# Optimization experiments

Hardware: AMD Instinct MI355X
Metric: run time of the kernel (lower is better)

Reference implementation:

```python
import jax, jax.numpy as jnp
import numpy as np

EMBED = 3072
HEADS = 24
HEAD_DIM = EMBED // HEADS
FFN = 4 * EMBED
SEGS = (1024, 2048, 4096)
DILS = (1, 2, 4)
SEQ = 8192
BATCH = 1


def setup_inputs() -> dict:
    key = jax.random.key(0)
    ks = jax.random.split(key, 8)
    E, F = EMBED, FFN
    s = lambda k, shape, sc: (jax.random.normal(k, shape, jnp.float32) * sc)
    return {
        "x": s(ks[0], (BATCH, SEQ, E), 1.0),
        "expert_embed": s(ks[1], (1, 1, E), 0.02),
        "w_qkv": s(ks[2], (3 * E, E), E ** -0.5),
        "b_qkv": jnp.zeros((3 * E,), jnp.float32),
        "w_out": s(ks[3], (E, E), E ** -0.5),
        "b_out": jnp.zeros((E,), jnp.float32),
        "ln1_g": jnp.ones((E,), jnp.float32),
        "ln1_b": jnp.zeros((E,), jnp.float32),
        "w1": s(ks[4], (F, E), E ** -0.5),
        "b1": jnp.zeros((F,), jnp.float32),
        "w2": s(ks[5], (E, F), F ** -0.5),
        "b2": jnp.zeros((E,), jnp.float32),
        "ln2_g": jnp.ones((E,), jnp.float32),
        "ln2_b": jnp.zeros((E,), jnp.float32),
    }


def _layernorm(x, g, b):
    m = jnp.mean(x, axis=-1, keepdims=True)
    v = jnp.mean(jnp.square(x - m), axis=-1, keepdims=True)
    return (x - m) * jax.lax.rsqrt(v + 1e-5) * g + b


def _dilated_attn(q, k, v):
    # q,k,v: [b, n, h, d]; heads are partitioned across dilation groups
    b, n, h, d = q.shape
    G = len(SEGS)
    hg = h // G
    scale = 1.0 / np.sqrt(d)
    outs = []
    for i, (g, r) in enumerate(zip(SEGS, DILS)):
        off = i % r
        hs = slice(i * hg, (i + 1) * hg)

        def sel(t):
            # [b, n, h, d] -> [b, n//g, g//r, hg, d] (dilated segment view)
            return t.reshape(b, n // g, g, h, d)[:, :, off::r, hs, :]

        qi, ki, vi = sel(q), sel(k), sel(v)
        att = jnp.einsum("bsqhd,bskhd->bshqk", qi, ki) * scale
        att = jax.nn.softmax(att, axis=-1)
        oi = jnp.einsum("bshqk,bskhd->bsqhd", att, vi)
        # scatter dilated positions back; unselected positions stay zero
        buf = jnp.zeros((b, n // g, g, hg, d), q.dtype).at[:, :, off::r].set(oi)
        outs.append(buf.reshape(b, n, hg, d))
    return jnp.concatenate(outs, axis=2)  # head groups are contiguous slices


def reference(x, expert_embed, w_qkv, b_qkv, w_out, b_out,
              ln1_g, ln1_b, w1, b1, w2, b2, ln2_g, ln2_b):
    b, n, E = x.shape
    x = x + expert_embed
    qkv = x @ w_qkv.T + b_qkv
    q, k, v = [t.reshape(b, n, HEADS, HEAD_DIM) for t in jnp.split(qkv, 3, axis=-1)]
    a = _dilated_attn(q, k, v).reshape(b, n, E) @ w_out.T + b_out
    x = _layernorm(x + a, ln1_g, ln1_b)
    f = jax.nn.gelu(x @ w1.T + b1, approximate=False) @ w2.T + b2
    return _layernorm(x + f, ln2_g, ln2_b)
```

## Files before the change

### kernel.cpp

```cpp
#include <hip/hip_runtime.h>

typedef unsigned short u16;
typedef __bf16 bf16x8 __attribute__((ext_vector_type(8)));
typedef float f32x4 __attribute__((ext_vector_type(4)));
typedef u16 u16x4 __attribute__((ext_vector_type(4)));
typedef u16 u16x8 __attribute__((ext_vector_type(8)));

__device__ __forceinline__ u16 f2bf(float f) {
  union { float f; unsigned u; } v; v.f = f;
  return (u16)((v.u + 0x7fffu + ((v.u >> 16) & 1u)) >> 16);
}
__device__ __forceinline__ float b2f(u16 h) {
  union { unsigned u; float f; } v; v.u = ((unsigned)h) << 16; return v.f;
}

__device__ __forceinline__ void gld16(const void* g, void* l) {
  __builtin_amdgcn_global_load_lds(
      (const __attribute__((address_space(1))) unsigned int*)g,
      (__attribute__((address_space(3))) unsigned int*)l, 16, 0, 0);
}

#define BAR() asm volatile("s_barrier" ::: "memory")
#define VMC4() asm volatile("s_waitcnt vmcnt(4)" ::: "memory")
#define VMC3() asm volatile("s_waitcnt vmcnt(3)" ::: "memory")
#define VMC0() asm volatile("s_waitcnt vmcnt(0)" ::: "memory")

__global__ __launch_bounds__(256) void prep_kernel(const float* __restrict__ x,
                                                   const float* __restrict__ ee,
                                                   u16* __restrict__ xb) {
  size_t i = ((size_t)blockIdx.x * 256 + threadIdx.x) * 4;
  int col = (int)(i % 3072);
  f32x4 v = *(const f32x4*)&x[i];
  f32x4 e = *(const f32x4*)&ee[col];
  v += e;
  u16x4 b = { f2bf(v[0]), f2bf(v[1]), f2bf(v[2]), f2bf(v[3]) };
  *(u16x4*)&xb[i] = b;
}

__global__ __launch_bounds__(256) void cvt_kernel(const float* __restrict__ in,
                                                  u16* __restrict__ out, size_t n) {
  size_t i = ((size_t)blockIdx.x * 256 + threadIdx.x) * 4;
  if (i >= n) return;
  f32x4 v = *(const f32x4*)&in[i];
  u16x4 b = { f2bf(v[0]), f2bf(v[1]), f2bf(v[2]), f2bf(v[3]) };
  *(u16x4*)&out[i] = b;
}

__global__ __launch_bounds__(256) void cvt_strided_kernel(const float* __restrict__ in,
                                                          u16* __restrict__ out, int k0) {
  size_t i = ((size_t)blockIdx.x * 256 + threadIdx.x) * 4;
  int n = (int)(i / 6144), k = (int)(i % 6144);
  f32x4 v = *(const f32x4*)&in[(size_t)n * 12288 + k0 + k];
  u16x4 b = { f2bf(v[0]), f2bf(v[1]), f2bf(v[2]), f2bf(v[3]) };
  *(u16x4*)&out[i] = b;
}

template<int EPI>
__global__ __launch_bounds__(512, 2) void gemm8_kernel(const u16* __restrict__ A,
                                                       const u16* __restrict__ B,
                                                       const float* __restrict__ bias,
                                                       void* __restrict__ C0,
                                                       void* __restrict__ C1,
                                                       int N, int K) {
  __shared__ __align__(16) u16 lds[65536];
  const int tid = threadIdx.x;
  const int lane = tid & 63;
  const int w = tid >> 6;
  const int lr = lane & 15, lc8 = (lane >> 4) * 8;
  const int wm128 = (w >> 2) * 128, wn64 = (w & 3) * 64;
  const int rsw = (lr & 7) << 3;

  const int ntile = N >> 8;
  int bid = blockIdx.x;
  int wg = (bid & 7) * (gridDim.x >> 3) + (bid >> 3);
  const int bm = wg / ntile, bn = wg % ntile;
  const size_t m0 = (size_t)bm << 8, n0 = (size_t)bn << 8;

  const int jsw = (tid & 7) ^ ((tid >> 3) & 7);
  const u16* gA = A + (m0 + (tid >> 3)) * (size_t)K + jsw * 8;
  const u16* gB = B + (n0 + ((tid >> 8) << 6) + ((tid >> 3) & 31)) * (size_t)K + jsw * 8;
  u16* lA = &lds[tid * 8];
  u16* lB = &lds[16384 + (((tid >> 8) << 12) | (((tid >> 3) & 31) << 6) | ((tid & 7) << 3))];

  f32x4 acc[8][4] = {};
  bf16x8 af[2][4], bfr[2][2];

  auto stageA = [&](int buf, int mh, int kk) {
    const int ro = mh * 64;
    gld16(gA + (size_t)ro * K + kk, lA + buf * 32768 + ro * 64);
    gld16(gA + (size_t)(ro + 128) * K + kk, lA + buf * 32768 + (ro + 128) * 64);
  };
  auto stageB = [&](int buf, int nh, int kk) {
    const int ro = nh * 32;
    gld16(gB + (size_t)ro * K + kk, lB + buf * 32768 + ro * 64);
    gld16(gB + (size_t)(ro + 128) * K + kk, lB + buf * 32768 + (ro + 128) * 64);
  };
  auto LA = [&](int buf, int mh) {
#pragma unroll
    for (int ks = 0; ks < 2; ++ks)
#pragma unroll
      for (int f = 0; f < 4; ++f) {
        int r = wm128 + mh * 64 + f * 16 + lr;
        af[ks][f] = *(const bf16x8*)&lds[buf * 32768 + r * 64 + ((ks * 32 + lc8) ^ rsw)];
      }
  };
  auto LB = [&](int buf, int nh) {
#pragma unroll
    for (int ks = 0; ks < 2; ++ks)
#pragma unroll
      for (int f = 0; f < 2; ++f) {
        int r = wn64 + nh * 32 + f * 16 + lr;
        bfr[ks][f] = *(const bf16x8*)&lds[buf * 32768 + 16384 + r * 64 + ((ks * 32 + lc8) ^ rsw)];
      }
  };
  auto MMA = [&](int mh, int nh) {
    __builtin_amdgcn_s_setprio(1);
#pragma unroll
    for (int ks = 0; ks < 2; ++ks)
#pragma unroll
      for (int f = 0; f < 4; ++f)
#pragma unroll
        for (int f2 = 0; f2 < 2; ++f2)
          acc[mh * 4 + f][nh * 2 + f2] = __builtin_amdgcn_mfma_f32_16x16x32_bf16(
              af[ks][f], bfr[ks][f2], acc[mh * 4 + f][nh * 2 + f2], 0, 0, 0);
    __builtin_amdgcn_s_setprio(0);
  };

  stageA(0, 0, 0); stageB(0, 1, 0); stageA(0, 1, 0); stageB(0, 0, 0);
  stageA(1, 0, 64); stageB(1, 1, 64);
  VMC4();
  BAR();

  const int NIT = K >> 7;
  for (int it = 0; it < NIT; ++it) {
    const int kk = it << 7;
    const bool pred = (it + 1 < NIT);
    LA(0, 0); LB(0, 0);
    stageA(1, 1, kk + 64);
    BAR(); MMA(0, 0); BAR();
    LB(0, 1);
    stageB(1, 0, kk + 64);
    BAR(); MMA(0, 1); BAR();
    LA(0, 1);
    if (pred) stageA(0, 0, kk + 128);
    BAR(); MMA(1, 1); BAR();
    LB(0, 0);
    if (pred) stageB(0, 1, kk + 128);
    BAR(); MMA(1, 0);
    if (pred) { VMC4(); } else { VMC0(); }
    BAR();
    LA(1, 0); LB(1, 0);
    if (pred) stageA(0, 1, kk + 128);
    BAR(); MMA(0, 0); BAR();
    LB(1, 1);
    if (pred) stageB(0, 0, kk + 128);
    BAR(); MMA(0, 1); BAR();
    LA(1, 1);
    if (pred) stageA(1, 0, kk + 192);
    BAR(); MMA(1, 1); BAR();
    LB(1, 0);
    if (pred) stageB(1, 1, kk + 192);
    BAR(); MMA(1, 0);
    if (pred) { VMC4(); }
    BAR();
  }

#pragma unroll
  for (int ni = 0; ni < 4; ++ni) {
    const int colL = wn64 + ni * 16 + lr;
    const size_t col = n0 + colL;
    const float bv = bias[col];
    const int ci = colL >> 3;
#pragma unroll
    for (int mi = 0; mi < 8; ++mi) {
#pragma unroll
      for (int rg = 0; rg < 4; ++rg) {
        const int rowL = wm128 + mi * 16 + (lc8 >> 1) + rg;
        float v = acc[mi][ni][rg] + bv;
        if constexpr (EPI == 2)
          v = 0.5f * v * (1.0f + erff(v * 0.7071067811865476f));
        const int fz = (rowL >> 2) & 7;
        lds[rowL * 256 + (((ci ^ fz) << 3) | (colL & 7))] = f2bf(v);
      }
    }
  }
  __syncthreads();
  const int row = tid >> 1, half = tid & 1;
  const int fro = (row >> 2) & 7;
  u16* dst;
  size_t cb;
  int ldc;
  if constexpr (EPI == 7) {
    const int sec = (n0 >= 3072);
    dst = sec ? (u16*)C1 : (u16*)C0;
    cb = n0 - (sec ? 3072 : 0);
    ldc = 3072;
  } else {
    dst = (u16*)C0; cb = n0; ldc = N;
  }
  u16* gout = dst + (m0 + row) * (size_t)ldc + cb + half * 128;
#pragma unroll
  for (int i = 0; i < 16; ++i) {
    const int ci = half * 16 + i;
    *(uint4*)&gout[i * 8] = *(const uint4*)&lds[row * 256 + ((ci ^ fro) << 3)];
  }
}

template<int EPI>
__global__ __launch_bounds__(512, 2) void gemm8n_kernel(const u16* __restrict__ A,
                                                        const u16* __restrict__ B,
                                                        const float* __restrict__ bias,
                                                        const float* __restrict__ residf,
                                                        const u16* __restrict__ residb,
                                                        const float* __restrict__ ee,
                                                        void* __restrict__ C0,
                                                        int N, int K) {
  __shared__ __align__(16) u16 lds[49152];
  const int tid = threadIdx.x;
  const int lane = tid & 63;
  const int w = tid >> 6;
  const int lr = lane & 15, lc8 = (lane >> 4) * 8;
  const int wm128 = (w >> 2) * 128;
  const int wn16 = (w & 3) * 16;
  const int rsw = (lr & 7) << 3;

  const int ntile = N >> 7;
  int bid = blockIdx.x;
  int wg = (bid & 7) * (gridDim.x >> 3) + (bid >> 3);
  const int bm = wg / ntile, bn = wg % ntile;
  const size_t m0 = (size_t)bm << 8, n0 = (size_t)bn << 7;

  const int jsw = (tid & 7) ^ ((tid >> 3) & 7);
  const u16* gA = A + (m0 + (tid >> 3)) * (size_t)K + jsw * 8;
  const u16* gB = B + (n0 + (tid >> 3)) * (size_t)K + jsw * 8;
  u16* lA = &lds[tid * 8];
  u16* lB = &lds[16384 + tid * 8];

  f32x4 acc[8][2] = {};
  bf16x8 af[2][4], bfr[2];

  auto stageA = [&](int buf, int mh, int kk) {
    const int ro = mh * 64;
    gld16(gA + (size_t)ro * K + kk, lA + buf * 24576 + ro * 64);
    gld16(gA + (size_t)(ro + 128) * K + kk, lA + buf * 24576 + (ro + 128) * 64);
  };
  auto stageB = [&](int buf, int nh, int kk) {
    gld16(gB + (size_t)(nh * 64) * K + kk, lB + buf * 24576 + nh * 4096);
  };
  auto LA = [&](int buf, int mh) {
#pragma unroll
    for (int ks = 0; ks < 2; ++ks)
#pragma unroll
      for (int f = 0; f < 4; ++f) {
        int r = wm128 + mh * 64 + f * 16 + lr;
        af[ks][f] = *(const bf16x8*)&lds[buf * 24576 + r * 64 + ((ks * 32 + lc8) ^ rsw)];
      }
  };
  auto LB = [&](int buf, int nh) {
#pragma unroll
    for (int ks = 0; ks < 2; ++ks) {
      int r = nh * 64 + wn16 + lr;
      bfr[ks] = *(const bf16x8*)&lds[buf * 24576 + 16384 + r * 64 + ((ks * 32 + lc8) ^ rsw)];
    }
  };
  auto MMA = [&](int mh, int nh) {
    __builtin_amdgcn_s_setprio(1);
#pragma unroll
    for (int ks = 0; ks < 2; ++ks)
#pragma unroll
      for (int f = 0; f < 4; ++f)
        acc[mh * 4 + f][nh] = __builtin_amdgcn_mfma_f32_16x16x32_bf16(
            af[ks][f], bfr[ks], acc[mh * 4 + f][nh], 0, 0, 0);
    __builtin_amdgcn_s_setprio(0);
  };

  stageA(0, 0, 0); stageB(0, 1, 0); stageA(0, 1, 0); stageB(0, 0, 0);
  stageA(1, 0, 64); stageB(1, 1, 64);
  VMC3();
  BAR();

  const int NIT = K >> 7;
  for (int it = 0; it < NIT; ++it) {
    const int kk = it << 7;
    const bool pred = (it + 1 < NIT);
    LA(0, 0); LB(0, 0);
    stageA(1, 1, kk + 64);
    BAR(); MMA(0, 0); BAR();
    LB(0, 1);
    stageB(1, 0, kk + 64);
    BAR(); MMA(0, 1); BAR();
    LA(0, 1);
    if (pred) stageA(0, 0, kk + 128);
    BAR(); MMA(1, 1); BAR();
    LB(0, 0);
    if (pred) stageB(0, 1, kk + 128);
    BAR(); MMA(1, 0);
    if (pred) { VMC3(); } else { VMC0(); }
    BAR();
    LA(1, 0); LB(1, 0);
    if (pred) stageA(0, 1, kk + 128);
    BAR(); MMA(0, 0); BAR();
    LB(1, 1);
    if (pred) stageB(0, 0, kk + 128);
    BAR(); MMA(0, 1); BAR();
    LA(1, 1);
    if (pred) stageA(1, 0, kk + 192);
    BAR(); MMA(1, 1); BAR();
    LB(1, 0);
    if (pred) stageB(1, 1, kk + 192);
    BAR(); MMA(1, 0);
    if (pred) { VMC3(); }
    BAR();
  }

#pragma unroll
  for (int nh = 0; nh < 2; ++nh) {
    const int colL = nh * 64 + wn16 + lr;
    const size_t col = n0 + colL;
    float bv = 0.f;
    if constexpr (EPI != 9) bv = bias[col];
    const int ci = colL >> 3;
#pragma unroll
    for (int mi = 0; mi < 8; ++mi) {
#pragma unroll
      for (int rg = 0; rg < 4; ++rg) {
        const int rowL = wm128 + mi * 16 + (lc8 >> 1) + rg;
        const size_t idx = (m0 + rowL) * (size_t)N + col;
        float v = acc[mi][nh][rg] + bv;
        if constexpr (EPI == 3) v += residf[idx] + ee[col];
        if constexpr (EPI == 8) v += b2f(residb[idx]);
        if constexpr (EPI == 9) v += b2f(((const u16*)C0)[idx]);
        const int fz = (rowL >> 2) & 7;
        lds[rowL * 128 + (((ci ^ fz) << 3) | (colL & 7))] = f2bf(v);
      }
    }
  }
  __syncthreads();
  const int row = tid >> 1, half = tid & 1;
  const int fro = (row >> 2) & 7;
  u16* gout = (u16*)C0 + (m0 + row) * (size_t)N + n0 + half * 64;
#pragma unroll
  for (int i = 0; i < 8; ++i) {
    const int ci = half * 8 + i;
    *(uint4*)&gout[i * 8] = *(const uint4*)&lds[row * 128 + ((ci ^ fro) << 3)];
  }
}

__device__ __forceinline__ void decode_blk(int bid, int& grp, int& g, int& r, int& off,
                                           int& q16, int& hl, int& s) {
  if (bid < 1024)      { grp = 0; g = 1024; r = 1; off = 0; }
  else if (bid < 1536) { grp = 1; g = 2048; r = 2; off = 1; bid -= 1024; }
  else                 { grp = 2; g = 4096; r = 4; off = 2; bid -= 1536; }
  q16 = bid & 15; hl = (bid >> 4) & 7; s = bid >> 7;
}

__global__ __launch_bounds__(256) void vtrans_kernel(const u16* __restrict__ Vb,
                                                     u16* __restrict__ vtd) {
  int grp, g, r, off, jb, hl, s;
  decode_blk(blockIdx.x, grp, g, r, off, jb, hl, s);
  const int h = grp * 8 + hl;
  const size_t vbase = (size_t)((grp == 0) ? 0u : (grp == 1) ? 8388608u : 12582912u)
                       + (size_t)(s * 8 + hl) * 131072;
  __shared__ u16 t[64 * 128];
  const int tid = threadIdx.x;
#pragma unroll
  for (int i = 0; i < 4; ++i) {
    int c = tid + i * 256;
    int jj = c >> 4, c16 = c & 15;
    size_t pos = (size_t)s * g + off + (size_t)(jb * 64 + jj) * r;
    uint4 d = *(const uint4*)&Vb[pos * 3072 + h * 128 + c16 * 8];
    *(uint4*)((char*)t + jj * 256 + ((c16 * 16) ^ ((jj >> 3) << 4))) = d;
  }
  __syncthreads();
#pragma unroll
  for (int i = 0; i < 4; ++i) {
    int c = tid + i * 256;
    int dd = c >> 3, jc = c & 7;
    u16x8 vals;
#pragma unroll
    for (int q = 0; q < 8; ++q) {
      int row = jc * 8 + q;
      vals[q] = *(const u16*)((const char*)t + row * 256 + ((dd * 2) ^ (jc << 4)));
    }
    *(u16x8*)&vtd[vbase + (size_t)dd * 1024 + jb * 64 + jc * 8] = vals;
  }
}

__global__ __launch_bounds__(256) void attn_kernel(const u16* __restrict__ Qb,
                                                   const u16* __restrict__ Kb,
                                                   const u16* __restrict__ vtd,
                                                   u16* __restrict__ abuf) {
  int grp, g, r, off, qt, hl, s;
  decode_blk(blockIdx.x, grp, g, r, off, qt, hl, s);
  const int h = grp * 8 + hl;
  const size_t vbase = (size_t)((grp == 0) ? 0u : (grp == 1) ? 8388608u : 12582912u)
                       + (size_t)(s * 8 + hl) * 131072;
  const size_t segoff = (size_t)s * g + off;

  const int tid = threadIdx.x;
  const int lane = tid & 63, w = tid >> 6;
  const int lr = lane & 15, lc = lane >> 4;

  __shared__ u16 Kl[64 * 128];
  __shared__ u16 Vl[128 * 64];
  __shared__ u16 Pl[4][1024];

  const size_t qpos = segoff + (size_t)(qt * 64 + w * 16 + lr) * r;
  const u16* qrow = &Qb[qpos * 3072 + h * 128];
  bf16x8 qf[4];
#pragma unroll
  for (int kc = 0; kc < 4; ++kc) qf[kc] = *(const bf16x8*)&qrow[kc * 32 + lc * 8];

  float m_run[4], l_run[4];
  f32x4 ao[8] = {};
#pragma unroll
  for (int i = 0; i < 4; ++i) { m_run[i] = -1e30f; l_run[i] = 0.f; }

  const float scale = 0.08838834764831845f;

  for (int kt = 0; kt < 16; ++kt) {
    __syncthreads();
#pragma unroll
    for (int i = 0; i < 4; ++i) {
      int c = tid + i * 256;
      int jj = c >> 4, c16 = c & 15;
      size_t kpos = segoff + (size_t)(kt * 64 + jj) * r;
      uint4 kd = *(const uint4*)&Kb[kpos * 3072 + h * 128 + c16 * 8];
      *(uint4*)((char*)Kl + jj * 256 + ((c16 * 16) ^ ((jj & 7) << 4))) = kd;
      int dd = c >> 3, jc = c & 7;
      uint4 vd = *(const uint4*)&vtd[vbase + (size_t)dd * 1024 + kt * 64 + jc * 8];
      *(uint4*)((char*)Vl + dd * 128 + ((jc * 16) ^ ((dd & 7) << 4))) = vd;
    }
    __syncthreads();

    f32x4 sc4[4] = {};
#pragma unroll
    for (int kb = 0; kb < 4; ++kb) {
      const int key = kb * 16 + lr;
      const int swz = (key & 7) << 4;
#pragma unroll
      for (int kc = 0; kc < 4; ++kc) {
        bf16x8 kf = *(const bf16x8*)((const char*)Kl + key * 256 + ((kc * 64 + lc * 16) ^ swz));
        sc4[kb] = __builtin_amdgcn_mfma_f32_16x16x32_bf16(qf[kc], kf, sc4[kb], 0, 0, 0);
      }
    }

    float pv[4][4];
#pragma unroll
    for (int rg = 0; rg < 4; ++rg) {
      float t = fmaxf(fmaxf(sc4[0][rg], sc4[1][rg]), fmaxf(sc4[2][rg], sc4[3][rg]));
#pragma unroll
      for (int sh = 1; sh < 16; sh <<= 1) t = fmaxf(t, __shfl_xor(t, sh, 64));
      t *= scale;
      const float mn = fmaxf(m_run[rg], t);
      const float corr = __expf(m_run[rg] - mn);
      m_run[rg] = mn;
      float sum = 0.f;
#pragma unroll
      for (int kb = 0; kb < 4; ++kb) {
        float p = __expf(sc4[kb][rg] * scale - mn);
        pv[kb][rg] = p; sum += p;
      }
#pragma unroll
      for (int sh = 1; sh < 16; sh <<= 1) sum += __shfl_xor(sum, sh, 64);
      l_run[rg] = l_run[rg] * corr + sum;
#pragma unroll
      for (int nb = 0; nb < 8; ++nb) ao[nb][rg] *= corr;
    }

#pragma unroll
    for (int rg = 0; rg < 4; ++rg) {
      const int q = lc * 4 + rg;
      const int swq = (q & 7) << 4;
#pragma unroll
      for (int kb = 0; kb < 4; ++kb) {
        const int key = kb * 16 + lr;
        *(u16*)((char*)&Pl[w][0] + q * 128 + ((key * 2) ^ swq)) = f2bf(pv[kb][rg]);
      }
    }
    __syncthreads();

#pragma unroll
    for (int kc2 = 0; kc2 < 2; ++kc2) {
      bf16x8 pf = *(const bf16x8*)((const char*)&Pl[w][0] + lr * 128 + ((kc2 * 64 + lc * 16) ^ ((lr & 7) << 4)));
#pragma unroll
      for (int nb = 0; nb < 8; ++nb) {
        const int dd = nb * 16 + lr;
        bf16x8 vf = *(const bf16x8*)((const char*)Vl + dd * 128 + ((kc2 * 64 + lc * 16) ^ ((dd & 7) << 4)));
        ao[nb] = __builtin_amdgcn_mfma_f32_16x16x32_bf16(pf, vf, ao[nb], 0, 0, 0);
      }
    }
  }

#pragma unroll
  for (int rg = 0; rg < 4; ++rg) {
    const float inv = 1.f / l_run[rg];
    const size_t opos = segoff + (size_t)(qt * 64 + w * 16 + lc * 4 + rg) * r;
    u16* orow = &abuf[opos * 3072 + h * 128];
#pragma unroll
    for (int nb = 0; nb < 8; ++nb) orow[nb * 16 + lr] = f2bf(ao[nb][rg] * inv);
  }
}

template<int IN_BF, int OUT_BF>
__global__ __launch_bounds__(256) void ln_kernel(const void* __restrict__ yv,
                                                 const float* __restrict__ gm,
                                                 const float* __restrict__ bt,
                                                 void* __restrict__ outv) {
  const size_t row = blockIdx.x;
  const int tid = threadIdx.x;
  float v[12];
  float s = 0.f, ss = 0.f;
#pragma unroll
  for (int i = 0; i < 3; ++i) {
    if constexpr (IN_BF) {
      u16x4 raw = *(const u16x4*)((const u16*)yv + row * 3072 + tid * 4 + i * 1024);
#pragma unroll
      for (int j = 0; j < 4; ++j) { float f = b2f(raw[j]); v[i * 4 + j] = f; s += f; ss += f * f; }
    } else {
      f32x4 raw = *(const f32x4*)((const float*)yv + row * 3072 + tid * 4 + i * 1024);
#pragma unroll
      for (int j = 0; j < 4; ++j) { float f = raw[j]; v[i * 4 + j] = f; s += f; ss += f * f; }
    }
  }
#pragma unroll
  for (int sh = 1; sh < 64; sh <<= 1) { s += __shfl_xor(s, sh, 64); ss += __shfl_xor(ss, sh, 64); }
  __shared__ float red[8];
  if ((tid & 63) == 0) { red[tid >> 6] = s; red[4 + (tid >> 6)] = ss; }
  __syncthreads();
  s = red[0] + red[1] + red[2] + red[3];
  ss = red[4] + red[5] + red[6] + red[7];
  const float mean = s * (1.f / 3072.f);
  const float var = ss * (1.f / 3072.f) - mean * mean;
  const float rs = rsqrtf(var + 1e-5f);
#pragma unroll
  for (int i = 0; i < 3; ++i) {
    int c = tid * 4 + i * 1024;
    f32x4 g4 = *(const f32x4*)&gm[c];
    f32x4 b4 = *(const f32x4*)&bt[c];
    if constexpr (OUT_BF) {
      u16x4 ob;
#pragma unroll
      for (int j = 0; j < 4; ++j) ob[j] = f2bf((v[i * 4 + j] - mean) * rs * g4[j] + b4[j]);
      *(u16x4*)((u16*)outv + row * 3072 + c) = ob;
    } else {
      f32x4 o;
#pragma unroll
      for (int j = 0; j < 4; ++j) o[j] = (v[i * 4 + j] - mean) * rs * g4[j] + b4[j];
      *(f32x4*)((float*)outv + row * 3072 + c) = o;
    }
  }
}

extern "C" void kernel_launch(void* const* d_in, const int* in_sizes, int n_in,
                              void* d_out, int out_size, void* d_ws, size_t ws_size,
                              hipStream_t stream) {
  (void)in_sizes; (void)n_in; (void)out_size;
  const float* x    = (const float*)d_in[0];
  const float* ee   = (const float*)d_in[1];
  const float* wqkv = (const float*)d_in[2];
  const float* bqkv = (const float*)d_in[3];
  const float* wout = (const float*)d_in[4];
  const float* bout = (const float*)d_in[5];
  const float* ln1g = (const float*)d_in[6];
  const float* ln1b = (const float*)d_in[7];
  const float* w1   = (const float*)d_in[8];
  const float* b1   = (const float*)d_in[9];
  const float* w2   = (const float*)d_in[10];
  const float* b2   = (const float*)d_in[11];
  const float* ln2g = (const float*)d_in[12];
  const float* ln2b = (const float*)d_in[13];
  float* out = (float*)d_out;

  static const size_t OFF_B1  = 50331648;
  static const size_t OFF_B2  = 100663296;
  static const size_t WS_NEED = 150994944;
  if (ws_size < WS_NEED) return;

  char* ws = (char*)d_ws;
  u16*   xb    = (u16*)(ws);
  u16*   vtd   = (u16*)(ws);
  u16*   wbo   = (u16*)(ws);
  u16*   x1b   = (u16*)(ws);
  u16*   Qb    = (u16*)(ws + OFF_B1);
  u16*   y1b   = (u16*)(ws + OFF_B1);
  u16*   y2b   = (u16*)(ws + OFF_B1);
  u16*   wslot = (u16*)(ws + OFF_B2);
  u16*   abuf  = (u16*)(ws + OFF_B2);
  u16*   Kb    = (u16*)d_out;
  u16*   Vb    = (u16*)((char*)d_out + 50331648);
  u16*   hcd   = (u16*)d_out;

  prep_kernel<<<24576, 256, 0, stream>>>(x, ee, xb);

  cvt_kernel<<<18432, 256, 0, stream>>>(wqkv, wslot, 18874368);
  gemm8_kernel<7><<<768, 512, 0, stream>>>(xb, wslot, bqkv, Qb, Kb, 6144, 3072);
  cvt_kernel<<<9216, 256, 0, stream>>>(wqkv + 18874368, wslot, 9437184);
  gemm8n_kernel<0><<<768, 512, 0, stream>>>(xb, wslot, bqkv + 6144, nullptr, nullptr, nullptr,
                                            Vb, 3072, 3072);

  vtrans_kernel<<<1792, 256, 0, stream>>>(Vb, vtd);
  hipMemsetAsync(abuf, 0, 50331648, stream);
  attn_kernel<<<1792, 256, 0, stream>>>(Qb, Kb, vtd, abuf);

  cvt_kernel<<<9216, 256, 0, stream>>>(wout, wbo, 9437184);
  gemm8n_kernel<3><<<768, 512, 0, stream>>>(abuf, wbo, bout, x, nullptr, ee,
                                            y1b, 3072, 3072);
  ln_kernel<1, 1><<<8192, 256, 0, stream>>>(y1b, ln1g, ln1b, x1b);

  for (int c = 0; c < 2; ++c) {
    cvt_kernel<<<18432, 256, 0, stream>>>(w1 + (size_t)c * 18874368, wslot, 18874368);
    gemm8_kernel<2><<<768, 512, 0, stream>>>(x1b, wslot, b1 + c * 6144, hcd, nullptr, 6144, 3072);
    cvt_strided_kernel<<<18432, 256, 0, stream>>>(w2, wslot, c * 6144);
    if (c == 0)
      gemm8n_kernel<8><<<768, 512, 0, stream>>>(hcd, wslot, b2, nullptr, x1b, nullptr,
                                                y2b, 3072, 6144);
    else
      gemm8n_kernel<9><<<768, 512, 0, stream>>>(hcd, wslot, b2, nullptr, nullptr, nullptr,
                                                y2b, 3072, 6144);
  }

  ln_kernel<1, 0><<<8192, 256, 0, stream>>>(y2b, ln2g, ln2b, out);
}
```

Before: 2.332 ms.

## Triple-buffer the N=3072 GEMM with 64x64 warp tiles and deepen prefetch

The 256x128 GEMM used for the V, out-projection and FFN-down GEMMs is replaced with a three-stage LDS ring buffer over 64-wide K slices. It also moves from 8 warps of 128x16 tiles to 4x2 warps of 64x64 tiles, which raises per-warp fragment reuse. The wider 8-wave GEMM reorders its async staging so one more stage is in flight, waiting at vmcnt(6) instead of vmcnt(4). The aim is to hide global-load latency and cut LDS fragment reloads. The larger LDS allocation (144 KB) likely stops two blocks from fitting per CU, reducing occupancy.

```diff
diff --git a/kernel.cpp b/kernel.cpp
--- a/kernel.cpp
+++ b/kernel.cpp
@@ -21,8 +21,7 @@
 }
 
 #define BAR() asm volatile("s_barrier" ::: "memory")
-#define VMC4() asm volatile("s_waitcnt vmcnt(4)" ::: "memory")
-#define VMC3() asm volatile("s_waitcnt vmcnt(3)" ::: "memory")
+#define VMC6() asm volatile("s_waitcnt vmcnt(6)" ::: "memory")
 #define VMC0() asm volatile("s_waitcnt vmcnt(0)" ::: "memory")
 
 __global__ __launch_bounds__(256) void prep_kernel(const float* __restrict__ x,
@@ -127,8 +126,8 @@
   };
 
   stageA(0, 0, 0); stageB(0, 1, 0); stageA(0, 1, 0); stageB(0, 0, 0);
-  stageA(1, 0, 64); stageB(1, 1, 64);
-  VMC4();
+  stageA(1, 0, 64); stageB(1, 1, 64); stageA(1, 1, 64);
+  VMC6();
   BAR();
 
   const int NIT = K >> 7;
@@ -136,32 +135,32 @@
     const int kk = it << 7;
     const bool pred = (it + 1 < NIT);
     LA(0, 0); LB(0, 0);
-    stageA(1, 1, kk + 64);
+    stageB(1, 0, kk + 64);
     BAR(); MMA(0, 0); BAR();
     LB(0, 1);
-    stageB(1, 0, kk + 64);
+    if (pred) stageA(0, 0, kk + 128);
     BAR(); MMA(0, 1); BAR();
     LA(0, 1);
-    if (pred) stageA(0, 0, kk + 128);
+    if (pred) stageB(0, 1, kk + 128);
     BAR(); MMA(1, 1); BAR();
     LB(0, 0);
-    if (pred) stageB(0, 1, kk + 128);
+    if (pred) stageA(0, 1, kk + 128);
     BAR(); MMA(1, 0);
-    if (pred) { VMC4(); } else { VMC0(); }
+    if (pred) { VMC6(); } else { VMC0(); }
     BAR();
     LA(1, 0); LB(1, 0);
-    if (pred) stageA(0, 1, kk + 128);
+    if (pred) stageB(0, 0, kk + 128);
     BAR(); MMA(0, 0); BAR();
     LB(1, 1);
-    if (pred) stageB(0, 0, kk + 128);
+    if (pred) stageA(1, 0, kk + 192);
     BAR(); MMA(0, 1); BAR();
     LA(1, 1);
-    if (pred) stageA(1, 0, kk + 192);
+    if (pred) stageB(1, 1, kk + 192);
     BAR(); MMA(1, 1); BAR();
     LB(1, 0);
-    if (pred) stageB(1, 1, kk + 192);
+    if (pred) stageA(1, 1, kk + 192);
     BAR(); MMA(1, 0);
-    if (pred) { VMC4(); }
+    if (pred) { VMC6(); }
     BAR();
   }
 
@@ -207,7 +206,7 @@
 }
 
 template<int EPI>
-__global__ __launch_bounds__(512, 2) void gemm8n_kernel(const u16* __restrict__ A,
+__global__ __launch_bounds__(512, 2) void gemm4p_kernel(const u16* __restrict__ A,
                                                         const u16* __restrict__ B,
                                                         const float* __restrict__ bias,
                                                         const float* __restrict__ residf,
@@ -215,13 +214,13 @@
                                                         const float* __restrict__ ee,
                                                         void* __restrict__ C0,
                                                         int N, int K) {
-  __shared__ __align__(16) u16 lds[49152];
+  __shared__ __align__(16) u16 lds[73728];
   const int tid = threadIdx.x;
   const int lane = tid & 63;
   const int w = tid >> 6;
   const int lr = lane & 15, lc8 = (lane >> 4) * 8;
-  const int wm128 = (w >> 2) * 128;
-  const int wn16 = (w & 3) * 16;
+  const int wm64 = (w >> 1) * 64;
+  const int wn64 = (w & 1) * 64;
   const int rsw = (lr & 7) << 3;
 
   const int ntile = N >> 7;
@@ -236,97 +235,89 @@
   u16* lA = &lds[tid * 8];
   u16* lB = &lds[16384 + tid * 8];
 
-  f32x4 acc[8][2] = {};
-  bf16x8 af[2][4], bfr[2];
-
-  auto stageA = [&](int buf, int mh, int kk) {
-    const int ro = mh * 64;
-    gld16(gA + (size_t)ro * K + kk, lA + buf * 24576 + ro * 64);
-    gld16(gA + (size_t)(ro + 128) * K + kk, lA + buf * 24576 + (ro + 128) * 64);
-  };
-  auto stageB = [&](int buf, int nh, int kk) {
-    gld16(gB + (size_t)(nh * 64) * K + kk, lB + buf * 24576 + nh * 4096);
-  };
-  auto LA = [&](int buf, int mh) {
+  f32x4 acc[4][4] = {};
+  bf16x8 af[2][4], bfr[2][2];
+
+  const int NT = K >> 6;
+
+  auto stageA2 = [&](int buf, int kk) {
+    gld16(gA + kk, lA + buf * 24576);
+    gld16(gA + (size_t)128 * K + kk, lA + buf * 24576 + 128 * 64);
+    gld16(gA + (size_t)64 * K + kk, lA + buf * 24576 + 64 * 64);
+    gld16(gA + (size_t)192 * K + kk, lA + buf * 24576 + 192 * 64);
+  };
+  auto stageB1 = [&](int buf, int kk) {
+    gld16(gB + kk, lB + buf * 24576);
+    gld16(gB + (size_t)64 * K + kk, lB + buf * 24576 + 64 * 64);
+  };
+  auto LA = [&](int buf) {
 #pragma unroll
     for (int ks = 0; ks < 2; ++ks)
 #pragma unroll
       for (int f = 0; f < 4; ++f) {
-        int r = wm128 + mh * 64 + f * 16 + lr;
+        int r = wm64 + f * 16 + lr;
         af[ks][f] = *(const bf16x8*)&lds[buf * 24576 + r * 64 + ((ks * 32 + lc8) ^ rsw)];
       }
   };
-  auto LB = [&](int buf, int nh) {
-#pragma unroll
-    for (int ks = 0; ks < 2; ++ks) {
-      int r = nh * 64 + wn16 + lr;
-      bfr[ks] = *(const bf16x8*)&lds[buf * 24576 + 16384 + r * 64 + ((ks * 32 + lc8) ^ rsw)];
-    }
-  };
-  auto MMA = [&](int mh, int nh) {
+  auto LB = [&](int buf, int ch) {
+#pragma unroll
+    for (int ks = 0; ks < 2; ++ks)
+#pragma unroll
+      for (int f2 = 0; f2 < 2; ++f2) {
+        int r = wn64 + ch * 32 + f2 * 16 + lr;
+        bfr[ks][f2] = *(const bf16x8*)&lds[buf * 24576 + 16384 + r * 64 + ((ks * 32 + lc8) ^ rsw)];
+      }
+  };
+  auto MMA = [&](int ch) {
     __builtin_amdgcn_s_setprio(1);
 #pragma unroll
     for (int ks = 0; ks < 2; ++ks)
 #pragma unroll
       for (int f = 0; f < 4; ++f)
-        acc[mh * 4 + f][nh] = __builtin_amdgcn_mfma_f32_16x16x32_bf16(
-            af[ks][f], bfr[ks], acc[mh * 4 + f][nh], 0, 0, 0);
+#pragma unroll
+        for (int f2 = 0; f2 < 2; ++f2)
+          acc[f][ch * 2 + f2] = __builtin_amdgcn_mfma_f32_16x16x32_bf16(
+              af[ks][f], bfr[ks][f2], acc[f][ch * 2 + f2], 0, 0, 0);
     __builtin_amdgcn_s_setprio(0);
   };
-
-  stageA(0, 0, 0); stageB(0, 1, 0); stageA(0, 1, 0); stageB(0, 0, 0);
-  stageA(1, 0, 64); stageB(1, 1, 64);
-  VMC3();
+  auto TILE = [&](int bc, int bs, int tt) {
+    const int kk2 = (tt + 2) << 6;
+    const bool p = (tt + 2) < NT;
+    LA(bc); LB(bc, 0);
+    if (p) stageA2(bs, kk2);
+    BAR(); MMA(0); BAR();
+    LB(bc, 1);
+    if (p) stageB1(bs, kk2);
+    BAR(); MMA(1);
+    if (p) { VMC6(); } else { VMC0(); }
+    BAR();
+  };
+
+  stageA2(0, 0); stageB1(0, 0);
+  stageA2(1, 64); stageB1(1, 64);
+  VMC6();
   BAR();
 
-  const int NIT = K >> 7;
-  for (int it = 0; it < NIT; ++it) {
-    const int kk = it << 7;
-    const bool pred = (it + 1 < NIT);
-    LA(0, 0); LB(0, 0);
-    stageA(1, 1, kk + 64);
-    BAR(); MMA(0, 0); BAR();
-    LB(0, 1);
-    stageB(1, 0, kk + 64);
-    BAR(); MMA(0, 1); BAR();
-    LA(0, 1);
-    if (pred) stageA(0, 0, kk + 128);
-    BAR(); MMA(1, 1); BAR();
-    LB(0, 0);
-    if (pred) stageB(0, 1, kk + 128);
-    BAR(); MMA(1, 0);
-    if (pred) { VMC3(); } else { VMC0(); }
-    BAR();
-    LA(1, 0); LB(1, 0);
-    if (pred) stageA(0, 1, kk + 128);
-    BAR(); MMA(0, 0); BAR();
-    LB(1, 1);
-    if (pred) stageB(0, 0, kk + 128);
-    BAR(); MMA(0, 1); BAR();
-    LA(1, 1);
-    if (pred) stageA(1, 0, kk + 192);
-    BAR(); MMA(1, 1); BAR();
-    LB(1, 0);
-    if (pred) stageB(1, 1, kk + 192);
-    BAR(); MMA(1, 0);
-    if (pred) { VMC3(); }
-    BAR();
-  }
-
-#pragma unroll
-  for (int nh = 0; nh < 2; ++nh) {
-    const int colL = nh * 64 + wn16 + lr;
+  for (int t = 0; t < NT; t += 3) {
+    TILE(0, 2, t);
+    TILE(1, 0, t + 1);
+    TILE(2, 1, t + 2);
+  }
+
+#pragma unroll
+  for (int nf = 0; nf < 4; ++nf) {
+    const int colL = wn64 + nf * 16 + lr;
     const size_t col = n0 + colL;
     float bv = 0.f;
     if constexpr (EPI != 9) bv = bias[col];
     const int ci = colL >> 3;
 #pragma unroll
-    for (int mi = 0; mi < 8; ++mi) {
+    for (int f = 0; f < 4; ++f) {
 #pragma unroll
       for (int rg = 0; rg < 4; ++rg) {
-        const int rowL = wm128 + mi * 16 + (lc8 >> 1) + rg;
+        const int rowL = wm64 + f * 16 + (lc8 >> 1) + rg;
         const size_t idx = (m0 + rowL) * (size_t)N + col;
-        float v = acc[mi][nh][rg] + bv;
+        float v = acc[f][nf][rg] + bv;
         if constexpr (EPI == 3) v += residf[idx] + ee[col];
         if constexpr (EPI == 8) v += b2f(residb[idx]);
         if constexpr (EPI == 9) v += b2f(((const u16*)C0)[idx]);
@@ -596,7 +587,7 @@
   cvt_kernel<<<18432, 256, 0, stream>>>(wqkv, wslot, 18874368);
   gemm8_kernel<7><<<768, 512, 0, stream>>>(xb, wslot, bqkv, Qb, Kb, 6144, 3072);
   cvt_kernel<<<9216, 256, 0, stream>>>(wqkv + 18874368, wslot, 9437184);
-  gemm8n_kernel<0><<<768, 512, 0, stream>>>(xb, wslot, bqkv + 6144, nullptr, nullptr, nullptr,
+  gemm4p_kernel<0><<<768, 512, 0, stream>>>(xb, wslot, bqkv + 6144, nullptr, nullptr, nullptr,
                                             Vb, 3072, 3072);
 
   vtrans_kernel<<<1792, 256, 0, stream>>>(Vb, vtd);
@@ -604,7 +595,7 @@
   attn_kernel<<<1792, 256, 0, stream>>>(Qb, Kb, vtd, abuf);
 
   cvt_kernel<<<9216, 256, 0, stream>>>(wout, wbo, 9437184);
-  gemm8n_kernel<3><<<768, 512, 0, stream>>>(abuf, wbo, bout, x, nullptr, ee,
+  gemm4p_kernel<3><<<768, 512, 0, stream>>>(abuf, wbo, bout, x, nullptr, ee,
                                             y1b, 3072, 3072);
   ln_kernel<1, 1><<<8192, 256, 0, stream>>>(y1b, ln1g, ln1b, x1b);
 
@@ -613,10 +604,10 @@
     gemm8_kernel<2><<<768, 512, 0, stream>>>(x1b, wslot, b1 + c * 6144, hcd, nullptr, 6144, 3072);
     cvt_strided_kernel<<<18432, 256, 0, stream>>>(w2, wslot, c * 6144);
     if (c == 0)
-      gemm8n_kernel<8><<<768, 512, 0, stream>>>(hcd, wslot, b2, nullptr, x1b, nullptr,
+      gemm4p_kernel<8><<<768, 512, 0, stream>>>(hcd, wslot, b2, nullptr, x1b, nullptr,
                                                 y2b, 3072, 6144);
     else
-      gemm8n_kernel<9><<<768, 512, 0, stream>>>(hcd, wslot, b2, nullptr, nullptr, nullptr,
+      gemm4p_kernel<9><<<768, 512, 0, stream>>>(hcd, wslot, b2, nullptr, nullptr, nullptr,
                                                 y2b, 3072, 6144);
   }
 
```

Result: faster. 2.253 ms (-3.4%).
